# Kernel optimization log

Hardware: AMD Instinct MI355X
Metric: run time of the kernel (lower is better)

The kernel has to match this reference:

```python
import jax, jax.numpy as jnp
import numpy as np

N_TOKEN = 400
N_LAYER = 12
N_HEAD = 8
D_MODEL = 512
D_FF = 2048
D_EMBED = 512
B = 4
S = 2048
HD = D_MODEL // N_HEAD
EPS = 1e-6


def sinusoidal_pe(seq_len, d):
    pos = np.arange(seq_len, dtype=np.float32)[:, None]
    div = np.exp(np.arange(0, d, 2, dtype=np.float32) * (-np.log(10000.0) / d))
    pe = np.zeros((seq_len, d), np.float32)
    pe[:, 0::2] = np.sin(pos * div)
    pe[:, 1::2] = np.cos(pos * div)
    return jnp.asarray(pe)


def layer_norm(x, g, b):
    m = jnp.mean(x, axis=-1, keepdims=True)
    v = jnp.var(x, axis=-1, keepdims=True)
    return (x - m) * jax.lax.rsqrt(v + 1e-5) * g + b


def causal_linear_attn(q, k, v):
    # q,k,v: [B,H,S,D]; FAVOR-style causal linear attention with elu+1 feature map
    q = jax.nn.elu(q) + 1.0
    k = jax.nn.elu(k) + 1.0
    qT = jnp.moveaxis(q, 2, 0)  # [S,B,H,D]
    kT = jnp.moveaxis(k, 2, 0)
    vT = jnp.moveaxis(v, 2, 0)
    Bq, H, _, D = q.shape
    init = (jnp.zeros((Bq, H, D, D), q.dtype), jnp.zeros((Bq, H, D), q.dtype))

    def step(carry, qkv):
        Sst, z = carry
        qi, ki, vi = qkv
        Sst = Sst + ki[..., :, None] * vi[..., None, :]  # running sum phi(k) v^T
        z = z + ki
        num = jnp.einsum('bhd,bhde->bhe', qi, Sst)
        den = jnp.einsum('bhd,bhd->bh', qi, z) + EPS
        return (Sst, z), num / den[..., None]

    _, out = jax.lax.scan(step, init, (qT, kT, vT))
    return jnp.moveaxis(out, 0, 2)  # [B,H,S,D]


def setup_inputs() -> dict:
    key = jax.random.key(0)
    ks = jax.random.split(key, 8)
    L = N_LAYER

    def nrm(k, shape, s=0.02):
        return jax.random.normal(k, shape, jnp.float32) * s

    return {
        'x': jax.random.randint(ks[0], (B, S), 0, N_TOKEN),
        'emb': nrm(ks[1], (N_TOKEN, D_EMBED)),
        'Wqkv': nrm(ks[2], (L, 3, D_MODEL, D_MODEL)),
        'bqkv': jnp.zeros((L, 3, D_MODEL), jnp.float32),
        'Wo': nrm(ks[3], (L, D_MODEL, D_MODEL)),
        'bo': jnp.zeros((L, D_MODEL), jnp.float32),
        'ln1_g': jnp.ones((L, D_MODEL), jnp.float32),
        'ln1_b': jnp.zeros((L, D_MODEL), jnp.float32),
        'W1': nrm(ks[4], (L, D_MODEL, D_FF)),
        'b1': jnp.zeros((L, D_FF), jnp.float32),
        'W2': nrm(ks[5], (L, D_FF, D_MODEL)),
        'b2': jnp.zeros((L, D_MODEL), jnp.float32),
        'ln2_g': jnp.ones((L, D_MODEL), jnp.float32),
        'ln2_b': jnp.zeros((L, D_MODEL), jnp.float32),
        'lnf_g': jnp.ones((D_MODEL,), jnp.float32),
        'lnf_b': jnp.zeros((D_MODEL,), jnp.float32),
        'Wout': nrm(ks[6], (D_MODEL, N_TOKEN)),
        'bout': jnp.zeros((N_TOKEN,), jnp.float32),
    }


def reference(x, emb, Wqkv, bqkv, Wo, bo, ln1_g, ln1_b, W1, b1, W2, b2,
              ln2_g, ln2_b, lnf_g, lnf_b, Wout, bout):
    # token embedding scaled by sqrt(d_model) + sinusoidal PE (dropout = eval identity)
    h = emb[x] * jnp.sqrt(jnp.float32(D_MODEL)) + sinusoidal_pe(S, D_EMBED)[None]

    def split_heads(t):  # [B,S,D_MODEL] -> [B,H,S,HD]
        return t.reshape(B, S, N_HEAD, HD).transpose(0, 2, 1, 3)

    for l in range(N_LAYER):
        q = split_heads(h @ Wqkv[l, 0] + bqkv[l, 0])
        k = split_heads(h @ Wqkv[l, 1] + bqkv[l, 1])
        v = split_heads(h @ Wqkv[l, 2] + bqkv[l, 2])
        a = causal_linear_attn(q, k, v)            # [B,H,S,HD]
        a = a.transpose(0, 2, 1, 3).reshape(B, S, D_MODEL)
        h = h + (a @ Wo[l] + bo[l])                # post-norm encoder layer
        h = layer_norm(h, ln1_g[l], ln1_b[l])
        y = jax.nn.relu(h @ W1[l] + b1[l]) @ W2[l] + b2[l]
        h = layer_norm(h + y, ln2_g[l], ln2_b[l])

    h = layer_norm(h, lnf_g, lnf_b)                # final norm from builder
    return h @ Wout + bout                         # [B,S,N_TOKEN]
```

## Files before the change

### kernel.cpp

```cpp
#include <hip/hip_runtime.h>
#include <hip/hip_bf16.h>

#define DM 512
#define DFF 2048
#define NB 4
#define SEQ 2048
#define NH 8
#define HD 64
#define NL 12
#define NT 400
#define MR (NB*SEQ)
#define CHK 64
#define NCH (SEQ/CHK)
#define NBH (NB*NH)
#define QS  (3*DM)
#define TP 72

typedef unsigned short u16;
typedef short bfrag __attribute__((ext_vector_type(8)));
typedef float ffrag __attribute__((ext_vector_type(4)));

__device__ __forceinline__ float bf2f(u16 u) { return __uint_as_float(((unsigned)u) << 16); }
__device__ __forceinline__ u16 f2bf(float f) {
    unsigned u = __float_as_uint(f);
    u += 0x7fffu + ((u >> 16) & 1u);
    return (u16)(u >> 16);
}

__device__ __forceinline__ void gload_lds16(const u16* g, u16* l) {
    __builtin_amdgcn_global_load_lds((const __attribute__((address_space(1))) void*)g,
                                     (__attribute__((address_space(3))) void*)l, 16, 0, 0);
}

__global__ __launch_bounds__(256) void wtr_kernel(const float* __restrict__ in,
                                                  u16* __restrict__ out,
                                                  int K, int N, int Nout)
{
    __shared__ float T[64][65];
    int n0 = blockIdx.x << 6, k0 = blockIdx.y << 6;
    const float* ip = in + (size_t)blockIdx.z * K * N;
    u16* op = out + (size_t)blockIdx.z * Nout * K;
    int c = threadIdx.x & 63, r = threadIdx.x >> 6;
#pragma unroll
    for (int i = 0; i < 16; ++i) {
        int k = k0 + 4 * i + r;
        int n = n0 + c;
        T[4 * i + r][c] = (n < N) ? ip[(size_t)k * N + n] : 0.f;
    }
    __syncthreads();
#pragma unroll
    for (int i = 0; i < 16; ++i) {
        int n = n0 + 4 * i + r;
        op[(size_t)n * K + k0 + c] = f2bf(T[c][4 * i + r]);
    }
}

__global__ __launch_bounds__(256) void embed_kernel(const int* __restrict__ x,
                                                    const float* __restrict__ emb,
                                                    float* __restrict__ h,
                                                    u16* __restrict__ hb)
{
    int row = blockIdx.x;
    int s = row & (SEQ - 1);
    int tok = x[row];
    int j = threadIdx.x;
    float2 ev = *(const float2*)(emb + (size_t)tok * DM + 2 * j);
    const float scale = 22.627416997969522f;
    float dv = expf((float)(2 * j) * (-9.210340371976184f / 512.0f));
    float ang = (float)s * dv;
    float2 o;
    o.x = ev.x * scale + sinf(ang);
    o.y = ev.y * scale + cosf(ang);
    *(float2*)(h + (size_t)row * DM + 2 * j) = o;
    ushort2 ob; ob.x = f2bf(o.x); ob.y = f2bf(o.y);
    *(ushort2*)(hb + (size_t)row * DM + 2 * j) = ob;
}

template<int BM>
__global__ __launch_bounds__(256) void mfma_gemm(
    const u16* __restrict__ A, const u16* __restrict__ Bt,
    const float* __restrict__ bias, const float* __restrict__ res,
    float* __restrict__ Cf, u16* __restrict__ Cb,
    int N, int K, int ldc, int Nw, int relu, int elu_cols)
{
    constexpr int ACH = BM / 16;
    constexpr int MI  = BM / 32;
    __shared__ __align__(16) u16 As[BM * 32];
    __shared__ __align__(16) u16 Bs[128 * 32];
    const int tid = threadIdx.x;
    const int w = tid >> 6, lane = tid & 63;
    const int m0 = blockIdx.x * BM, n0 = blockIdx.y << 7;
    const int wm = (w >> 1) * (BM / 2), wn = (w & 1) << 6;
    const int row16 = lane & 15, kq = lane >> 4;
    const int srow = lane >> 2;
    const int skoff = (lane & 3) << 3;

    ffrag acc[MI][4] = {};

    for (int k0 = 0; k0 < K; k0 += 32) {
#pragma unroll
        for (int q = 0; q < (ACH + 8) / 4; ++q) {
            int ci = w + (q << 2);
            if (ci < ACH) {
                gload_lds16(A  + (size_t)(m0 + (ci << 4) + srow) * K + k0 + skoff, As + (ci << 9));
            } else {
                int cb = ci - ACH;
                gload_lds16(Bt + (size_t)(n0 + (cb << 4) + srow) * K + k0 + skoff, Bs + (cb << 9));
            }
        }
        __syncthreads();
        bfrag af[MI], bfq[4];
#pragma unroll
        for (int i = 0; i < MI; ++i)
            af[i]  = *(const bfrag*)(As + ((wm + (i << 4) + row16) << 5) + (kq << 3));
#pragma unroll
        for (int j = 0; j < 4; ++j)
            bfq[j] = *(const bfrag*)(Bs + ((wn + (j << 4) + row16) << 5) + (kq << 3));
#pragma unroll
        for (int i = 0; i < MI; ++i)
#pragma unroll
            for (int j = 0; j < 4; ++j)
                acc[i][j] = __builtin_amdgcn_mfma_f32_16x16x32_bf16(af[i], bfq[j], acc[i][j], 0, 0, 0);
        __syncthreads();
    }

    const int crow = (lane >> 4) << 2;
    const int ccol = lane & 15;
#pragma unroll
    for (int i = 0; i < MI; ++i) {
        int mg = m0 + wm + (i << 4) + crow;
#pragma unroll
        for (int j = 0; j < 4; ++j) {
            int ng = n0 + wn + (j << 4) + ccol;
            if (ng < Nw) {
                float bsv = bias[ng];
#pragma unroll
                for (int r = 0; r < 4; ++r) {
                    float v = acc[i][j][r] + bsv;
                    size_t idx = (size_t)(mg + r) * ldc + ng;
                    if (res) v += res[idx];
                    if (relu) v = fmaxf(v, 0.f);
                    if (ng < elu_cols) v = (v > 0.f) ? v + 1.f : __expf(v);
                    if (Cf) Cf[idx] = v;
                    if (Cb) Cb[idx] = f2bf(v);
                }
            }
        }
    }
}

__global__ __launch_bounds__(256) void chunksum_kernel(
    const u16* __restrict__ qkv, float* __restrict__ Ssum, float* __restrict__ zsum)
{
    __shared__ __align__(16) u16 KT[64 * TP];
    __shared__ __align__(16) u16 VT[64 * TP];
    int blk = blockIdx.x;
    int c = blk % NCH; int bh = blk / NCH;
    int hh = bh % NH;  int b = bh / NH;
    const u16* kbase = qkv + ((size_t)b * SEQ + (size_t)c * CHK) * QS + DM + hh * HD;
    const u16* vbase = kbase + DM;
    const int tid = threadIdx.x;
    const int w = tid >> 6, lane = tid & 63;
    const int col = lane & 15, quad = lane >> 4;

    {
        int t = tid >> 2, d0 = (tid & 3) << 4;
        bfrag k0 = *(const bfrag*)(kbase + (size_t)t * QS + d0);
        bfrag k1 = *(const bfrag*)(kbase + (size_t)t * QS + d0 + 8);
        bfrag v0 = *(const bfrag*)(vbase + (size_t)t * QS + d0);
        bfrag v1 = *(const bfrag*)(vbase + (size_t)t * QS + d0 + 8);
#pragma unroll
        for (int i = 0; i < 8; ++i) {
            KT[(d0 + i) * TP + t] = (u16)k0[i];
            KT[(d0 + 8 + i) * TP + t] = (u16)k1[i];
            VT[(d0 + i) * TP + t] = (u16)v0[i];
            VT[(d0 + 8 + i) * TP + t] = (u16)v1[i];
        }
    }
    __syncthreads();

    bfrag ktf[2];
#pragma unroll
    for (int kk = 0; kk < 2; ++kk)
        ktf[kk] = *(const bfrag*)(KT + ((w << 4) + col) * TP + kk * 32 + (quad << 3));
    bfrag ones;
#pragma unroll
    for (int i = 0; i < 8; ++i) ones[i] = (short)0x3F80;

    ffrag acc[4] = {};
    ffrag zacc = {};
#pragma unroll
    for (int j = 0; j < 4; ++j)
#pragma unroll
        for (int kk = 0; kk < 2; ++kk) {
            bfrag vf = *(const bfrag*)(VT + ((j << 4) + col) * TP + kk * 32 + (quad << 3));
            acc[j] = __builtin_amdgcn_mfma_f32_16x16x32_bf16(ktf[kk], vf, acc[j], 0, 0, 0);
        }
    zacc = __builtin_amdgcn_mfma_f32_16x16x32_bf16(ktf[0], ones, zacc, 0, 0, 0);
    zacc = __builtin_amdgcn_mfma_f32_16x16x32_bf16(ktf[1], ones, zacc, 0, 0, 0);

    float* So = Ssum + (size_t)blk * (HD * HD);
#pragma unroll
    for (int j = 0; j < 4; ++j)
#pragma unroll
        for (int r = 0; r < 4; ++r)
            So[((w << 4) + (quad << 2) + r) * HD + (j << 4) + col] = acc[j][r];
    if (col == 0) {
#pragma unroll
        for (int r = 0; r < 4; ++r)
            zsum[(size_t)blk * HD + (w << 4) + (quad << 2) + r] = zacc[r];
    }
}

__global__ __launch_bounds__(256) void prefix_kernel(float* __restrict__ Ssum,
                                                     float* __restrict__ zsum)
{
    int bh = blockIdx.x >> 4;
    int eg = blockIdx.x & 15;
    int entry = (eg << 8) + threadIdx.x;
    size_t base = (size_t)bh * NCH * (HD * HD) + entry;
    float pre = 0.f;
    for (int c = 0; c < NCH; ++c) {
        float cur = Ssum[base + (size_t)c * (HD * HD)];
        Ssum[base + (size_t)c * (HD * HD)] = pre;
        pre += cur;
    }
    if (eg == 0 && threadIdx.x < 64) {
        size_t zb = (size_t)bh * NCH * HD + threadIdx.x;
        float zp = 0.f;
        for (int c = 0; c < NCH; ++c) {
            float cur = zsum[zb + c * HD];
            zsum[zb + c * HD] = zp;
            zp += cur;
        }
    }
}

__global__ __launch_bounds__(256) void attn_kernel(
    const u16* __restrict__ qkv, const float* __restrict__ Spre,
    const float* __restrict__ zpre, u16* __restrict__ ab)
{
    __shared__ __align__(16) u16 Qs[64 * 64];
    __shared__ __align__(16) u16 KP[64 * TP];
    __shared__ __align__(16) u16 VT[64 * TP];
    __shared__ __align__(16) u16 SpT[64 * TP];
    __shared__ __align__(16) u16 zb[64];
    int blk = blockIdx.x;
    int c = blk % NCH; int bh = blk / NCH;
    int hh = bh % NH;  int b = bh / NH;
    const int tid = threadIdx.x;
    const int w = tid >> 6, lane = tid & 63;
    const int col = lane & 15, quad = lane >> 4;
    const size_t rowbase = ((size_t)b * SEQ + (size_t)c * CHK);
    const u16* qbase = qkv + rowbase * QS + hh * HD;
    const u16* vbase = qbase + 2 * DM;

#pragma unroll
    for (int li = 0; li < 2; ++li) {
        int ld = (li << 2) + w;
        int grow = (ld << 3) + (lane >> 3);
        int gcol = (lane & 7) << 3;
        gload_lds16(qbase + (size_t)grow * QS + gcol, Qs + (ld << 9));
        gload_lds16(qbase + DM + (size_t)grow * QS + gcol, KP + (ld << 9));
    }
    {
        int t = tid >> 2, e0 = (tid & 3) << 4;
        bfrag v0 = *(const bfrag*)(vbase + (size_t)t * QS + e0);
        bfrag v1 = *(const bfrag*)(vbase + (size_t)t * QS + e0 + 8);
#pragma unroll
        for (int i = 0; i < 8; ++i) {
            VT[(e0 + i) * TP + t] = (u16)v0[i];
            VT[(e0 + 8 + i) * TP + t] = (u16)v1[i];
        }
    }
    {
        const float* sp = Spre + ((size_t)bh * NCH + c) * (HD * HD);
        int d = tid >> 2, e0 = (tid & 3) << 4;
#pragma unroll
        for (int g = 0; g < 4; ++g) {
            float4 f = *(const float4*)(sp + d * HD + e0 + (g << 2));
            SpT[(e0 + (g << 2) + 0) * TP + d] = f2bf(f.x);
            SpT[(e0 + (g << 2) + 1) * TP + d] = f2bf(f.y);
            SpT[(e0 + (g << 2) + 2) * TP + d] = f2bf(f.z);
            SpT[(e0 + (g << 2) + 3) * TP + d] = f2bf(f.w);
        }
    }
    if (tid < 64) zb[tid] = f2bf(zpre[((size_t)bh * NCH + c) * HD + tid]);
    __syncthreads();

    bfrag qf[2];
#pragma unroll
    for (int kk = 0; kk < 2; ++kk)
        qf[kk] = *(const bfrag*)(Qs + ((w << 4) + col) * 64 + kk * 32 + (quad << 3));

    ffrag S[4] = {};
#pragma unroll
    for (int j = 0; j < 4; ++j)
#pragma unroll
        for (int kk = 0; kk < 2; ++kk) {
            bfrag kf = *(const bfrag*)(KP + ((j << 4) + col) * 64 + kk * 32 + (quad << 3));
            S[j] = __builtin_amdgcn_mfma_f32_16x16x32_bf16(qf[kk], kf, S[j], 0, 0, 0);
        }
    __syncthreads();

    float rs[4] = {0.f, 0.f, 0.f, 0.f};
#pragma unroll
    for (int j = 0; j < 4; ++j)
#pragma unroll
        for (int r = 0; r < 4; ++r) {
            int t = (w << 4) + (quad << 2) + r;
            int u = (j << 4) + col;
            float sv = (u <= t) ? S[j][r] : 0.f;
            rs[r] += sv;
            KP[t * TP + u] = f2bf(sv);
        }
#pragma unroll
    for (int r = 0; r < 4; ++r) {
        rs[r] += __shfl_xor(rs[r], 1);
        rs[r] += __shfl_xor(rs[r], 2);
        rs[r] += __shfl_xor(rs[r], 4);
        rs[r] += __shfl_xor(rs[r], 8);
    }

    ffrag dacc = {};
#pragma unroll
    for (int kk = 0; kk < 2; ++kk) {
        bfrag zf = *(const bfrag*)(zb + kk * 32 + (quad << 3));
        dacc = __builtin_amdgcn_mfma_f32_16x16x32_bf16(qf[kk], zf, dacc, 0, 0, 0);
    }

    ffrag O[4] = {};
    bfrag pf[2];
#pragma unroll
    for (int kk = 0; kk < 2; ++kk)
        pf[kk] = *(const bfrag*)(KP + ((w << 4) + col) * TP + kk * 32 + (quad << 3));
#pragma unroll
    for (int j = 0; j < 4; ++j)
#pragma unroll
        for (int kk = 0; kk < 2; ++kk) {
            bfrag sf = *(const bfrag*)(SpT + ((j << 4) + col) * TP + kk * 32 + (quad << 3));
            O[j] = __builtin_amdgcn_mfma_f32_16x16x32_bf16(qf[kk], sf, O[j], 0, 0, 0);
            bfrag vf = *(const bfrag*)(VT + ((j << 4) + col) * TP + kk * 32 + (quad << 3));
            O[j] = __builtin_amdgcn_mfma_f32_16x16x32_bf16(pf[kk], vf, O[j], 0, 0, 0);
        }

#pragma unroll
    for (int j = 0; j < 4; ++j)
#pragma unroll
        for (int r = 0; r < 4; ++r) {
            int t = (w << 4) + (quad << 2) + r;
            int e = (j << 4) + col;
            float den = dacc[r] + rs[r] + 1e-6f;
            ab[(rowbase + t) * DM + hh * HD + e] = f2bf(O[j][r] / den);
        }
}

__global__ __launch_bounds__(256) void ln_kernel(
    const float* __restrict__ in, const float* __restrict__ gg,
    const float* __restrict__ bb, float* __restrict__ out, u16* __restrict__ outb)
{
    __shared__ float red[8];
    int row = blockIdx.x, tid = threadIdx.x;
    const float* xp = in + (size_t)row * DM;
    float2 xv = *(const float2*)(xp + 2 * tid);
    float s = xv.x + xv.y;
    float sq = xv.x * xv.x + xv.y * xv.y;
#pragma unroll
    for (int off = 32; off > 0; off >>= 1) {
        s  += __shfl_down(s, off);
        sq += __shfl_down(sq, off);
    }
    if ((tid & 63) == 0) { red[tid >> 6] = s; red[4 + (tid >> 6)] = sq; }
    __syncthreads();
    float st = red[0] + red[1] + red[2] + red[3];
    float sqt = red[4] + red[5] + red[6] + red[7];
    float m = st * (1.0f / DM);
    float var = sqt * (1.0f / DM) - m * m;
    float rs = rsqrtf(var + 1e-5f);
    float2 o;
    o.x = (xv.x - m) * rs * gg[2 * tid]     + bb[2 * tid];
    o.y = (xv.y - m) * rs * gg[2 * tid + 1] + bb[2 * tid + 1];
    *(float2*)(out + (size_t)row * DM + 2 * tid) = o;
    ushort2 ob; ob.x = f2bf(o.x); ob.y = f2bf(o.y);
    *(ushort2*)(outb + (size_t)row * DM + 2 * tid) = ob;
}

extern "C" void kernel_launch(void* const* d_in, const int* in_sizes, int n_in,
                              void* d_out, int out_size, void* d_ws, size_t ws_size,
                              hipStream_t stream)
{
    (void)in_sizes; (void)n_in; (void)out_size; (void)ws_size;
    const int*   x    = (const int*)d_in[0];
    const float* emb  = (const float*)d_in[1];
    const float* Wqkv = (const float*)d_in[2];
    const float* bqkv = (const float*)d_in[3];
    const float* Wo   = (const float*)d_in[4];
    const float* bo   = (const float*)d_in[5];
    const float* ln1g = (const float*)d_in[6];
    const float* ln1b = (const float*)d_in[7];
    const float* W1   = (const float*)d_in[8];
    const float* b1   = (const float*)d_in[9];
    const float* W2   = (const float*)d_in[10];
    const float* b2   = (const float*)d_in[11];
    const float* ln2g = (const float*)d_in[12];
    const float* ln2b = (const float*)d_in[13];
    const float* lnfg = (const float*)d_in[14];
    const float* lnfb = (const float*)d_in[15];
    const float* Wout = (const float*)d_in[16];
    const float* bout = (const float*)d_in[17];

    char* p = (char*)d_ws;
    float* h     = (float*)p;  p += (size_t)MR * DM * 4;
    u16*  hb     = (u16*)p;    p += (size_t)MR * DM * 2;
    u16*  qkvb   = (u16*)p;    p += (size_t)MR * QS * 2;
    u16*  abb    = (u16*)p;    p += (size_t)MR * DM * 2;
    u16*  midb   = (u16*)p;    p += (size_t)MR * DFF * 2;
    float* Ssum  = (float*)p;  p += (size_t)NBH * NCH * HD * HD * 4;
    float* zsum  = (float*)p;  p += (size_t)NBH * NCH * HD * 4;
    u16* WqkvT   = (u16*)p;    p += (size_t)NL * 3 * DM * DM * 2;
    u16* WoT     = (u16*)p;    p += (size_t)NL * DM * DM * 2;
    u16* W1T     = (u16*)p;    p += (size_t)NL * DFF * DM * 2;
    u16* W2T     = (u16*)p;    p += (size_t)NL * DM * DFF * 2;
    u16* WoutT   = (u16*)p;    p += (size_t)DM * DM * 2;

    wtr_kernel<<<dim3(8, 8, NL * 3), 256, 0, stream>>>(Wqkv, WqkvT, DM, DM, DM);
    wtr_kernel<<<dim3(8, 8, NL), 256, 0, stream>>>(Wo, WoT, DM, DM, DM);
    wtr_kernel<<<dim3(32, 8, NL), 256, 0, stream>>>(W1, W1T, DM, DFF, DFF);
    wtr_kernel<<<dim3(8, 32, NL), 256, 0, stream>>>(W2, W2T, DFF, DM, DM);
    wtr_kernel<<<dim3(8, 8, 1), 256, 0, stream>>>(Wout, WoutT, DM, NT, DM);

    embed_kernel<<<MR, 256, 0, stream>>>(x, emb, h, hb);

    for (int l = 0; l < NL; ++l) {
        mfma_gemm<128><<<dim3(MR / 128, QS / 128), 256, 0, stream>>>(
            hb, WqkvT + (size_t)l * QS * DM, bqkv + (size_t)l * QS, nullptr,
            nullptr, qkvb, QS, DM, QS, QS, 0, 2 * DM);

        chunksum_kernel<<<NBH * NCH, 256, 0, stream>>>(qkvb, Ssum, zsum);
        prefix_kernel<<<NBH * 16, 256, 0, stream>>>(Ssum, zsum);
        attn_kernel<<<NBH * NCH, 256, 0, stream>>>(qkvb, Ssum, zsum, abb);

        mfma_gemm<64><<<dim3(MR / 64, DM / 128), 256, 0, stream>>>(
            abb, WoT + (size_t)l * DM * DM, bo + (size_t)l * DM, h,
            h, nullptr, DM, DM, DM, DM, 0, 0);
        ln_kernel<<<MR, 256, 0, stream>>>(h, ln1g + (size_t)l * DM, ln1b + (size_t)l * DM, h, hb);

        mfma_gemm<128><<<dim3(MR / 128, DFF / 128), 256, 0, stream>>>(
            hb, W1T + (size_t)l * DFF * DM, b1 + (size_t)l * DFF, nullptr,
            nullptr, midb, DFF, DM, DFF, DFF, 1, 0);
        mfma_gemm<64><<<dim3(MR / 64, DM / 128), 256, 0, stream>>>(
            midb, W2T + (size_t)l * DM * DFF, b2 + (size_t)l * DM, h,
            h, nullptr, DM, DFF, DM, DM, 0, 0);
        ln_kernel<<<MR, 256, 0, stream>>>(h, ln2g + (size_t)l * DM, ln2b + (size_t)l * DM, h, hb);
    }

    ln_kernel<<<MR, 256, 0, stream>>>(h, lnfg, lnfb, h, hb);
    mfma_gemm<64><<<dim3(MR / 64, DM / 128), 256, 0, stream>>>(
        hb, WoutT, bout, nullptr, (float*)d_out, nullptr, DM, DM, NT, NT, 0, 0);
}
```

Before: 2.469 ms.

## Register-prefetch next K tile in GEMM and double K step to 64

Replaces direct global-to-LDS loads in the MFMA GEMM with loads into registers that prefetch the next K tile while the current tile is being computed, and widens the K step from 32 to 64 by splitting LDS into two 32-wide planes. The goal is to hide global memory latency behind MFMA work and halve the number of barriers per K pass. In exchange it uses more registers and LDS, which may lower occupancy, and it assumes K is a multiple of 64.

```diff
diff --git a/kernel.cpp b/kernel.cpp
--- a/kernel.cpp
+++ b/kernel.cpp
@@ -83,44 +83,74 @@
     float* __restrict__ Cf, u16* __restrict__ Cb,
     int N, int K, int ldc, int Nw, int relu, int elu_cols)
 {
-    constexpr int ACH = BM / 16;
-    constexpr int MI  = BM / 32;
-    __shared__ __align__(16) u16 As[BM * 32];
-    __shared__ __align__(16) u16 Bs[128 * 32];
+    constexpr int MI = BM / 32;
+    constexpr int AE = BM * 64 / (256 * 8);
+    constexpr int PA = BM * 32;
+    constexpr int PB = 128 * 32;
+    __shared__ __align__(16) u16 As[BM * 64];
+    __shared__ __align__(16) u16 Bs[128 * 64];
     const int tid = threadIdx.x;
     const int w = tid >> 6, lane = tid & 63;
     const int m0 = blockIdx.x * BM, n0 = blockIdx.y << 7;
     const int wm = (w >> 1) * (BM / 2), wn = (w & 1) << 6;
     const int row16 = lane & 15, kq = lane >> 4;
-    const int srow = lane >> 2;
-    const int skoff = (lane & 3) << 3;
 
     ffrag acc[MI][4] = {};
-
-    for (int k0 = 0; k0 < K; k0 += 32) {
-#pragma unroll
-        for (int q = 0; q < (ACH + 8) / 4; ++q) {
-            int ci = w + (q << 2);
-            if (ci < ACH) {
-                gload_lds16(A  + (size_t)(m0 + (ci << 4) + srow) * K + k0 + skoff, As + (ci << 9));
-            } else {
-                int cb = ci - ACH;
-                gload_lds16(Bt + (size_t)(n0 + (cb << 4) + srow) * K + k0 + skoff, Bs + (cb << 9));
+    bfrag aR[AE], bR[4];
+
+#pragma unroll
+    for (int j = 0; j < AE; ++j) {
+        int o = j * 2048 + 8 * tid;
+        int row = (o & (PA - 1)) >> 5;
+        int col = ((o / PA) << 5) + (o & 31);
+        aR[j] = *(const bfrag*)(A + (size_t)(m0 + row) * K + col);
+    }
+#pragma unroll
+    for (int j = 0; j < 4; ++j) {
+        int o = j * 2048 + 8 * tid;
+        int row = (o & (PB - 1)) >> 5;
+        int col = ((o / PB) << 5) + (o & 31);
+        bR[j] = *(const bfrag*)(Bt + (size_t)(n0 + row) * K + col);
+    }
+
+    for (int k0 = 0; k0 < K; k0 += 64) {
+#pragma unroll
+        for (int j = 0; j < AE; ++j) *(bfrag*)(As + j * 2048 + 8 * tid) = aR[j];
+#pragma unroll
+        for (int j = 0; j < 4; ++j)  *(bfrag*)(Bs + j * 2048 + 8 * tid) = bR[j];
+        __syncthreads();
+        if (k0 + 64 < K) {
+            int kn = k0 + 64;
+#pragma unroll
+            for (int j = 0; j < AE; ++j) {
+                int o = j * 2048 + 8 * tid;
+                int row = (o & (PA - 1)) >> 5;
+                int col = ((o / PA) << 5) + (o & 31);
+                aR[j] = *(const bfrag*)(A + (size_t)(m0 + row) * K + kn + col);
             }
-        }
-        __syncthreads();
-        bfrag af[MI], bfq[4];
-#pragma unroll
-        for (int i = 0; i < MI; ++i)
-            af[i]  = *(const bfrag*)(As + ((wm + (i << 4) + row16) << 5) + (kq << 3));
-#pragma unroll
-        for (int j = 0; j < 4; ++j)
-            bfq[j] = *(const bfrag*)(Bs + ((wn + (j << 4) + row16) << 5) + (kq << 3));
-#pragma unroll
-        for (int i = 0; i < MI; ++i)
+#pragma unroll
+            for (int j = 0; j < 4; ++j) {
+                int o = j * 2048 + 8 * tid;
+                int row = (o & (PB - 1)) >> 5;
+                int col = ((o / PB) << 5) + (o & 31);
+                bR[j] = *(const bfrag*)(Bt + (size_t)(n0 + row) * K + kn + col);
+            }
+        }
+#pragma unroll
+        for (int kk = 0; kk < 2; ++kk) {
+            bfrag af[MI], bfq[4];
+#pragma unroll
+            for (int i = 0; i < MI; ++i)
+                af[i]  = *(const bfrag*)(As + kk * PA + ((wm + (i << 4) + row16) << 5) + (kq << 3));
 #pragma unroll
             for (int j = 0; j < 4; ++j)
-                acc[i][j] = __builtin_amdgcn_mfma_f32_16x16x32_bf16(af[i], bfq[j], acc[i][j], 0, 0, 0);
+                bfq[j] = *(const bfrag*)(Bs + kk * PB + ((wn + (j << 4) + row16) << 5) + (kq << 3));
+#pragma unroll
+            for (int i = 0; i < MI; ++i)
+#pragma unroll
+                for (int j = 0; j < 4; ++j)
+                    acc[i][j] = __builtin_amdgcn_mfma_f32_16x16x32_bf16(af[i], bfq[j], acc[i][j], 0, 0, 0);
+        }
         __syncthreads();
     }
 
```

After: 2.268 ms. -8.2%, faster.
